# Kernel optimization log

Hardware: AMD Instinct MI355X
Metric: run time of the kernel (lower is better)

The kernel has to match this reference:

```python
import jax, jax.numpy as jnp
import numpy as np

DIM = 64; N_LAYER = 2; B = 2048; M = 64
N_ENT = 100000; N_REL = 200
TEMP = 0.2; KGE_W = 1e-6
MIN_N = 1e-15; BND = 1e-5


def _norm(x):
    return jnp.sqrt(jnp.clip((x * x).sum(-1, keepdims=True), MIN_N))


def _l2(x):
    # F.normalize(p=2): x / max(||x||, 1e-12)
    return x / jnp.maximum(jnp.sqrt((x * x).sum(-1, keepdims=True)), 1e-12)


def _artanh(x):
    return jnp.arctanh(jnp.clip(x, -1.0 + BND, 1.0 - BND))


def expmap0(u):
    n = _norm(u)
    return jnp.tanh(n) * u / n


def logmap0(x):
    n = _norm(x)
    return _artanh(n) * x / n


def mobius_add(x, y):
    x2 = (x * x).sum(-1, keepdims=True)
    y2 = (y * y).sum(-1, keepdims=True)
    xy = (x * y).sum(-1, keepdims=True)
    num = (1 + 2 * xy + y2) * x + (1 - x2) * y
    den = 1 + 2 * xy + x2 * y2
    return num / jnp.clip(den, MIN_N)


def expmap(u, p):
    lam = 2.0 / jnp.clip(1.0 - (p * p).sum(-1, keepdims=True), MIN_N)
    n = _norm(u)
    return mobius_add(p, jnp.tanh(lam * n / 2.0) * u / n)


def logmap(x, p):
    m = mobius_add(-p, x)
    n = _norm(m)
    lam = 2.0 / jnp.clip(1.0 - (p * p).sum(-1, keepdims=True), MIN_N)
    return (2.0 / lam) * _artanh(n) * m / n


def _ed_agg(h, path, t, att_w1, att_w2):
    # attention: Linear(2d,d,no bias) -> LeakyReLU(0)==ReLU -> Linear(d,1,no bias) -> Sigmoid
    x = jnp.concatenate([h, path], -1)                       # [B,M,2d]
    a = jax.nn.sigmoid(jax.nn.relu(x @ att_w1) @ att_w2)[..., 0]  # [B,M]
    w = jax.nn.softmax(a, axis=-1)
    return (w[..., None] * t).sum(1)                          # [B,d]


def _hyper_agg(h, path, t, curvature, a2_w1, a2_b1, a2_w2, a2_b2):
    h, path, t = _l2(h), _l2(path), _l2(t)
    hh = expmap0(h) * jnp.abs(curvature)
    ht = expmap(t, hh)
    hr = expmap(path, hh)
    tang = logmap0(jnp.concatenate([hh, hr], -1))            # [B,M,2d]
    a = jnp.tanh(jax.nn.relu(tang @ a2_w1 + a2_b1) @ a2_w2 + a2_b2)[..., 0]
    w = jax.nn.softmax(a, axis=-1)                            # [B,M]
    agg = w[..., None] * ht
    mean_pt = (w[..., None] * hh).sum(1, keepdims=True)       # [B,1,d]
    e = logmap(agg, mean_pt)
    return (w[..., None] * e).sum(1)                          # [B,d]


def _build(E, R, h_idx, r_idx, t_idx, init_emb, agg):
    embs = [init_emb]
    for i in range(N_LAYER):
        h = E[h_idx[0]]
        path = R[r_idx[0]]
        for k in range(1, i + 1):  # faithful to source: inner loop reuses index i
            h = h + E[h_idx[i]]
            path = path * R[r_idx[i]]
        embs.append(agg(h, path, E[t_idx[i]]))
    return jnp.stack(embs)  # [L+1, B, d]


def _mlcl(a_stack, b_stack):
    # vectorized over layer index i of MLCL_Loss(a[i], b[i], a_list, b_list)
    na, nb = _l2(a_stack), _l2(b_stack)                       # [L+1,B,d]
    d = na.shape[-1]
    pos = (na * nb).sum(-1)                                   # [L+1,B]
    ttl1 = jnp.einsum('lbd,md->lbm', na, nb.reshape(-1, d))
    ttl2 = jnp.einsum('lbd,md->lbm', nb, na.reshape(-1, d))
    ep = jnp.exp(pos / TEMP)
    l1 = -jnp.log(ep / jnp.exp(ttl1 / TEMP).sum(-1)).sum()
    l2 = -jnp.log(ep / jnp.exp(ttl2 / TEMP).sum(-1)).sum()
    return KGE_W * (l1 + l2)


def _cat_rev(stack):
    # e = stack[0]; for i in 1..L: e = cat(stack[i], e) -> [L, L-1, ..., 0]
    return jnp.concatenate([stack[i] for i in range(stack.shape[0] - 1, -1, -1)], -1)


def setup_inputs() -> dict:
    key = jax.random.key(0)
    ks = jax.random.split(key, 24)
    def ent_idx(k):
        return jax.random.randint(k, (N_LAYER, B, M), 0, N_ENT, dtype=jnp.int32)
    def rel_idx(k):
        return jax.random.randint(k, (N_LAYER, B, M), 0, N_REL, dtype=jnp.int32)
    inp = {
        'items': jax.random.randint(ks[0], (B,), 0, N_ENT, dtype=jnp.int32),
        'ucf_h': ent_idx(ks[1]), 'ucf_r': rel_idx(ks[2]), 'ucf_t': ent_idx(ks[3]),
        'ikg_h': ent_idx(ks[4]), 'ikg_r': rel_idx(ks[5]), 'ikg_t': ent_idx(ks[6]),
        'ukg_h': ent_idx(ks[7]), 'ukg_r': rel_idx(ks[8]), 'ukg_t': ent_idx(ks[9]),
        'icf_h': ent_idx(ks[10]), 'icf_r': rel_idx(ks[11]), 'icf_t': ent_idx(ks[12]),
        'ent_emb': jax.random.normal(ks[13], (N_ENT, DIM), jnp.float32) * 0.02,
        'rel_emb': jax.random.normal(ks[14], (N_REL, DIM), jnp.float32) * 0.02,
        'att_w1': jax.random.normal(ks[15], (2 * DIM, DIM), jnp.float32) * 0.05,
        'att_w2': jax.random.normal(ks[16], (DIM, 1), jnp.float32) * 0.05,
        'att2_w1': jax.random.normal(ks[17], (2 * DIM, DIM), jnp.float32) * 0.05,
        'att2_b1': jnp.zeros((DIM,), jnp.float32),
        'att2_w2': jax.random.normal(ks[18], (DIM, 1), jnp.float32) * 0.05,
        'att2_b2': jnp.zeros((1,), jnp.float32),
        'curvature': jnp.asarray(1.0, jnp.float32),
    }
    return inp


def reference(items, ucf_h, ucf_r, ucf_t, ikg_h, ikg_r, ikg_t,
              ukg_h, ukg_r, ukg_t, icf_h, icf_r, icf_t,
              ent_emb, rel_emb, att_w1, att_w2,
              att2_w1, att2_b1, att2_w2, att2_b2, curvature):
    ed = lambda h, p, t: _ed_agg(h, p, t, att_w1, att_w2)
    hy = lambda h, p, t: _hyper_agg(h, p, t, curvature, att2_w1, att2_b1, att2_w2, att2_b2)
    ucf = _build(ent_emb, rel_emb, ucf_h, ucf_r, ucf_t, ent_emb[ucf_h[0]].mean(1), ed)
    ikg = _build(ent_emb, rel_emb, ikg_h, ikg_r, ikg_t, ent_emb[items], ed)
    ukg = _build(ent_emb, rel_emb, ukg_h, ukg_r, ukg_t, ent_emb[ukg_h[0]].mean(1), hy)
    icf = _build(ent_emb, rel_emb, icf_h, icf_r, icf_t, ent_emb[icf_h[0]].mean(1), hy)
    kge_loss = _mlcl(ucf, ukg) + _mlcl(ikg, icf)
    e_u = jnp.concatenate([_cat_rev(ucf), _cat_rev(ukg)], -1)
    e_i = jnp.concatenate([_cat_rev(icf), _cat_rev(ikg)], -1)
    scores = jax.nn.sigmoid((e_i * e_u).sum(-1))
    return scores, kge_loss
```

## Files before the change

### kernel.cpp

```cpp
#include <hip/hip_runtime.h>
#include <hip/hip_bf16.h>
#include <cstdint>
#include <cstddef>

constexpr int NB = 2048;
constexpr int NM = 64;
constexpr int ND = 64;
constexpr int NBM = NB * NM;
constexpr int NROWS = 3 * NB;
constexpr int STACK = 3 * NB * ND;
constexpr int NZ = 8;

typedef __attribute__((ext_vector_type(8))) short short8;
typedef __attribute__((ext_vector_type(4))) float float4v;

__device__ __forceinline__ float wsum(float v) {
#pragma unroll
  for (int o = 32; o > 0; o >>= 1) v += __shfl_xor(v, o, 64);
  return v;
}

__device__ __forceinline__ float wmax(float v) {
#pragma unroll
  for (int o = 32; o > 0; o >>= 1) v = fmaxf(v, __shfl_xor(v, o, 64));
  return v;
}

__device__ __forceinline__ float rcpf(float x) { return __builtin_amdgcn_rcpf(x); }
__device__ __forceinline__ float sqf(float x) { return __builtin_amdgcn_sqrtf(x); }

__device__ __forceinline__ float fast_tanh(float x) {
  float t = __expf(2.f * x);
  return (t - 1.f) * rcpf(t + 1.f);
}

__device__ __forceinline__ float artanh_clip(float x) {
  x = fminf(fmaxf(x, -1.f + 1e-5f), 1.f - 1e-5f);
  return 0.5f * __logf((1.f + x) * rcpf(1.f - x));
}

__device__ __forceinline__ ushort f2bf(float f) {
  return (ushort)((__float_as_uint(f) + 0x8000u) >> 16);
}
__device__ __forceinline__ float bf2f(ushort u) {
  return __uint_as_float((uint)u << 16);
}
__device__ __forceinline__ uint pack_bf2(float h, float p) {
  uint hu = __float_as_uint(h) + 0x8000u;
  uint pu = __float_as_uint(p) + 0x8000u;
  return __builtin_amdgcn_perm(pu, hu, 0x07060302);
}
__device__ __forceinline__ float hp_lo(uint v) { return __uint_as_float(v << 16); }
__device__ __forceinline__ float hp_hi(uint v) { return __uint_as_float(v & 0xFFFF0000u); }

__device__ __forceinline__ float readlane_f(float v, int l) {
  return __int_as_float(__builtin_amdgcn_readlane(__float_as_int(v), l));
}

__global__ __launch_bounds__(256) void pack_w1_kernel(
    const float* __restrict__ w1, ushort* __restrict__ out) {
  int e = blockIdx.x * 256 + threadIdx.x;
  if (e >= 8192) return;
  int j = e & 7, ln = (e >> 3) & 63, nt = (e >> 9) & 3, kt = e >> 11;
  int n = nt * 16 + (ln & 15), k = kt * 32 + ((ln >> 4) << 3) + j;
  out[e] = f2bf(w1[k * 64 + n]);
}

__global__ __launch_bounds__(64) void init_item_kernel(
    const float* __restrict__ E, const int* __restrict__ idx, float* __restrict__ out) {
  int b = blockIdx.x, lane = threadIdx.x;
  out[(size_t)b * ND + lane] = E[(size_t)idx[b] * ND + lane];
}

constexpr int OFF_H = 0;
constexpr int OFF_P = 4608;
constexpr int OFF_T = 9728;
constexpr int XS = 152;
constexpr int REGA_SZ = 14336;

__global__ __launch_bounds__(256) void agg_all_kernel(
    const float* __restrict__ E, const float* __restrict__ R,
    const int* __restrict__ h0, const int* __restrict__ r0, const int* __restrict__ t0,
    const int* __restrict__ h1, const int* __restrict__ r1, const int* __restrict__ t1,
    const int* __restrict__ h2, const int* __restrict__ r2, const int* __restrict__ t2,
    const int* __restrict__ h3, const int* __restrict__ r3, const int* __restrict__ t3,
    const ushort* __restrict__ w1p_ed, const float* __restrict__ w2_ed,
    const ushort* __restrict__ w1p_hy, const float* __restrict__ b1,
    const float* __restrict__ w2_hy, const float* __restrict__ b2,
    const float* __restrict__ curv,
    float* __restrict__ s_ucf, float* __restrict__ s_ikg,
    float* __restrict__ s_ukg, float* __restrict__ s_icf) {
  __shared__ __align__(16) ushort regA[REGA_SZ];
  __shared__ float a_s[64];
  __shared__ float part[4][64];
  __shared__ float minit[4][64];

  const int b = blockIdx.x;
  const int fam = blockIdx.y;
  const int tid = threadIdx.x;
  const int wave = tid >> 6, lane = tid & 63;
  const int m0 = __builtin_amdgcn_readfirstlane(wave) * 16;
  const int colq = lane & 15, quad = lane >> 4;
  const size_t L = (size_t)NB * ND;

  const int* h_idx = (fam == 0) ? h0 : (fam == 1) ? h1 : (fam == 2) ? h2 : h3;
  const int* r_idx = (fam == 0) ? r0 : (fam == 1) ? r1 : (fam == 2) ? r2 : r3;
  const int* t_idx = (fam == 0) ? t0 : (fam == 1) ? t1 : (fam == 2) ? t2 : t3;
  float* sb = (fam == 0) ? s_ucf : (fam == 1) ? s_ikg : (fam == 2) ? s_ukg : s_icf;

  uint hp[16];

  if (fam < 2) {
    const int do_init = (fam == 0);
    for (int layer = 0; layer < 2; ++layer) {
      float tv[16];
      if (layer == 0) {
        float macc = 0.f;
#pragma unroll
        for (int mi = 0; mi < 16; ++mi) {
          const int m = m0 + mi;
          float hd = E[(size_t)h_idx[b * NM + m] * ND + lane];
          float pd = R[(size_t)r_idx[b * NM + m] * ND + lane];
          macc += hd;
          uint pk = pack_bf2(hd, pd);
          hp[mi] = pk;
          regA[m * XS + lane] = (ushort)pk;
          regA[m * XS + 64 + lane] = (ushort)(pk >> 16);
        }
        if (do_init) minit[wave][lane] = macc;
      } else {
#pragma unroll
        for (int mi = 0; mi < 16; ++mi) {
          const int m = m0 + mi;
          float hd = hp_lo(hp[mi]) + E[(size_t)h_idx[NBM + b * NM + m] * ND + lane];
          float pd = hp_hi(hp[mi]) * R[(size_t)r_idx[NBM + b * NM + m] * ND + lane];
          uint pk = pack_bf2(hd, pd);
          hp[mi] = pk;
          regA[m * XS + lane] = (ushort)pk;
          regA[m * XS + 64 + lane] = (ushort)(pk >> 16);
        }
      }
#pragma unroll
      for (int mi = 0; mi < 16; ++mi)
        tv[mi] = E[(size_t)t_idx[(size_t)layer * NBM + b * NM + m0 + mi] * ND + lane];

      {
        short8 afr[4];
#pragma unroll
        for (int kt = 0; kt < 4; ++kt)
          afr[kt] = *(const short8*)&regA[(m0 + colq) * XS + kt * 32 + quad * 8];
        float w2v[4];
#pragma unroll
        for (int nt = 0; nt < 4; ++nt) w2v[nt] = w2_ed[nt * 16 + colq];
        float cc[4][4];
#pragma unroll
        for (int nt = 0; nt < 4; ++nt) {
          float4v c = {0.f, 0.f, 0.f, 0.f};
#pragma unroll
          for (int kt = 0; kt < 4; ++kt) {
            short8 bfr = *(const short8*)&w1p_ed[(((kt << 2) | nt) * 64 + lane) * 8];
            c = __builtin_amdgcn_mfma_f32_16x16x32_bf16(afr[kt], bfr, c, 0, 0, 0);
          }
#pragma unroll
          for (int i = 0; i < 4; ++i) cc[nt][i] = c[i];
        }
        float sred[4];
#pragma unroll
        for (int i = 0; i < 4; ++i)
          sred[i] = fmaxf(cc[0][i], 0.f) * w2v[0] + fmaxf(cc[1][i], 0.f) * w2v[1] +
                    fmaxf(cc[2][i], 0.f) * w2v[2] + fmaxf(cc[3][i], 0.f) * w2v[3];
#pragma unroll
        for (int o = 8; o > 0; o >>= 1) {
#pragma unroll
          for (int i = 0; i < 4; ++i) sred[i] += __shfl_xor(sred[i], o, 64);
        }
        if (colq == 0) {
#pragma unroll
          for (int i = 0; i < 4; ++i)
            a_s[m0 + quad * 4 + i] = 1.f / (1.f + __expf(-sred[i]));
        }
      }
      __syncthreads();

      float wl;
      {
        float v = a_s[lane];
        float mx = wmax(v);
        float e = __expf(v - mx);
        wl = e / wsum(e);
      }
      if (layer == 0 && do_init && wave == 0)
        sb[(size_t)b * ND + lane] =
            (minit[0][lane] + minit[1][lane] + minit[2][lane] + minit[3][lane]) * (1.f / 64.f);

      float o = 0.f;
#pragma unroll
      for (int mi = 0; mi < 16; ++mi)
        o = fmaf(readlane_f(wl, m0 + mi), tv[mi], o);
      part[wave][lane] = o;
      __syncthreads();
      if (wave == 0)
        sb[(layer + 1) * L + (size_t)b * ND + lane] =
            part[0][lane] + part[1][lane] + part[2][lane] + part[3][lane];
    }
  } else {
    const float cabs = fabsf(*curv);
    const int j = colq;
    const int srcl = ((j >> 2) << 4) + j;

    for (int layer = 0; layer < 2; ++layer) {
      if (layer == 0) {
        float macc = 0.f;
#pragma unroll
        for (int mi = 0; mi < 16; ++mi) {
          const int m = m0 + mi;
          float hd = E[(size_t)h_idx[b * NM + m] * ND + lane];
          float pd = R[(size_t)r_idx[b * NM + m] * ND + lane];
          float td = E[(size_t)t_idx[b * NM + m] * ND + lane];
          macc += hd;
          uint pk = pack_bf2(hd, pd);
          hp[mi] = pk;
          regA[OFF_H + m * 72 + lane] = (ushort)pk;
          regA[OFF_P + m * 72 + lane] = (ushort)(pk >> 16);
          regA[OFF_T + m * 72 + lane] = f2bf(td);
        }
        part[wave][lane] = macc;
      } else {
#pragma unroll
        for (int mi = 0; mi < 16; ++mi) {
          const int m = m0 + mi;
          float hd = hp_lo(hp[mi]) + E[(size_t)h_idx[NBM + b * NM + m] * ND + lane];
          float pd = hp_hi(hp[mi]) * R[(size_t)r_idx[NBM + b * NM + m] * ND + lane];
          float td = E[(size_t)t_idx[(size_t)NBM + b * NM + m] * ND + lane];
          uint pk = pack_bf2(hd, pd);
          hp[mi] = pk;
          regA[OFF_H + m * 72 + lane] = (ushort)pk;
          regA[OFF_P + m * 72 + lane] = (ushort)(pk >> 16);
          regA[OFF_T + m * 72 + lane] = f2bf(td);
        }
      }

      float sh, sp, st, sht, shp;
      {
        const int fr = m0 + colq;
        const ushort* pH = &regA[OFF_H + fr * 72 + quad * 8];
        const ushort* pP = &regA[OFF_P + fr * 72 + quad * 8];
        const ushort* pT = &regA[OFF_T + fr * 72 + quad * 8];
        short8 hh0 = *(const short8*)pH, hh1 = *(const short8*)(pH + 32);
        short8 pp0 = *(const short8*)pP, pp1 = *(const short8*)(pP + 32);
        short8 tt0 = *(const short8*)pT, tt1 = *(const short8*)(pT + 32);
        const int dr = colq & 3;
#define DIAG_DOT(OUTV, A0, A1, B0, B1)                                      \
        {                                                                    \
          float4v c = {0.f, 0.f, 0.f, 0.f};                                  \
          c = __builtin_amdgcn_mfma_f32_16x16x32_bf16(A0, B0, c, 0, 0, 0);   \
          c = __builtin_amdgcn_mfma_f32_16x16x32_bf16(A1, B1, c, 0, 0, 0);   \
          float dv = (dr & 2) ? ((dr & 1) ? c[3] : c[2])                     \
                              : ((dr & 1) ? c[1] : c[0]);                    \
          OUTV = __shfl(dv, srcl, 64);                                       \
        }
        DIAG_DOT(sh, hh0, hh1, hh0, hh1)
        DIAG_DOT(sp, pp0, pp1, pp0, pp1)
        DIAG_DOT(st, tt0, tt1, tt0, tt1)
        DIAG_DOT(sht, hh0, hh1, tt0, tt1)
        DIAG_DOT(shp, hh0, hh1, pp0, pp1)
#undef DIAG_DOT
      }

      float g_ch, g_e1, g_e2, g_gh, g_q1, g_q2, g_hts2;
      {
        float rih = rcpf(fmaxf(sqf(sh), 1e-12f));
        float rip = rcpf(fmaxf(sqf(sp), 1e-12f));
        float rit = rcpf(fmaxf(sqf(st), 1e-12f));
        float nh = sqf(fmaxf(sh * rih * rih, 1e-15f));
        float ch = fast_tanh(nh) * rcpf(nh) * rih * cabs;
        float p2 = ch * ch * sh;
        float lam = 2.f * rcpf(fmaxf(1.f - p2, 1e-15f));
        float ntn = sqf(fmaxf(st * rit * rit, 1e-15f));
        float ct = fast_tanh(0.5f * lam * ntn) * rcpf(ntn) * rit;
        float y2 = ct * ct * st, xy = ch * ct * sht;
        float At = 1.f + 2.f * xy + y2, Bt = 1.f - p2;
        float rdt = rcpf(fmaxf(1.f + 2.f * xy + p2 * y2, 1e-15f));
        g_e1 = At * ch * rdt;
        g_e2 = Bt * ct * rdt;
        g_hts2 = g_e1 * g_e1 * sh + 2.f * g_e1 * g_e2 * sht + g_e2 * g_e2 * st;
        float npn = sqf(fmaxf(sp * rip * rip, 1e-15f));
        float cp = fast_tanh(0.5f * lam * npn) * rcpf(npn) * rip;
        float z2 = cp * cp * sp, xz = ch * cp * shp;
        float Ar = 1.f + 2.f * xz + z2;
        float rdr = rcpf(fmaxf(1.f + 2.f * xz + p2 * z2, 1e-15f));
        float f1 = Ar * ch * rdr, f2 = Bt * cp * rdr;
        float hr2 = f1 * f1 * sh + 2.f * f1 * f2 * shp + f2 * f2 * sp;
        float n128 = sqf(fmaxf(p2 + hr2, 1e-15f));
        float fq = artanh_clip(n128) * rcpf(n128);
        g_ch = ch;
        g_gh = fq * ch;
        g_q1 = fq * f1;
        g_q2 = fq * f2;
      }

      __syncthreads();
      if (layer == 0 && wave == 0)
        sb[(size_t)b * ND + lane] =
            (part[0][lane] + part[1][lane] + part[2][lane] + part[3][lane]) * (1.f / 64.f);

#pragma unroll
      for (int mi = 0; mi < 16; ++mi) {
        const int m = m0 + mi;
        float hvf = hp_lo(hp[mi]);
        float pvf = hp_hi(hp[mi]);
        float tvf = bf2f(regA[OFF_T + m * 72 + lane]);
        float ghm = readlane_f(g_gh, mi);
        float q1m = readlane_f(g_q1, mi);
        float q2m = readlane_f(g_q2, mi);
        float e1m = readlane_f(g_e1, mi);
        float e2m = readlane_f(g_e2, mi);
        regA[m * XS + lane] = f2bf(ghm * hvf);
        regA[m * XS + 64 + lane] = f2bf(q1m * hvf + q2m * pvf);
        regA[OFF_T + m * 72 + lane] = f2bf(e1m * hvf + e2m * tvf);
      }

      {
        short8 afr[4];
#pragma unroll
        for (int kt = 0; kt < 4; ++kt)
          afr[kt] = *(const short8*)&regA[(m0 + colq) * XS + kt * 32 + quad * 8];
        float b1v[4], w2v[4];
#pragma unroll
        for (int nt = 0; nt < 4; ++nt) {
          b1v[nt] = b1[nt * 16 + colq];
          w2v[nt] = w2_hy[nt * 16 + colq];
        }
        float cc[4][4];
#pragma unroll
        for (int nt = 0; nt < 4; ++nt) {
          float4v c = {0.f, 0.f, 0.f, 0.f};
#pragma unroll
          for (int kt = 0; kt < 4; ++kt) {
            short8 bfr = *(const short8*)&w1p_hy[(((kt << 2) | nt) * 64 + lane) * 8];
            c = __builtin_amdgcn_mfma_f32_16x16x32_bf16(afr[kt], bfr, c, 0, 0, 0);
          }
#pragma unroll
          for (int i = 0; i < 4; ++i) cc[nt][i] = c[i];
        }
        float b2v = b2[0];
        float sred[4];
#pragma unroll
        for (int i = 0; i < 4; ++i)
          sred[i] = fmaxf(cc[0][i] + b1v[0], 0.f) * w2v[0] +
                    fmaxf(cc[1][i] + b1v[1], 0.f) * w2v[1] +
                    fmaxf(cc[2][i] + b1v[2], 0.f) * w2v[2] +
                    fmaxf(cc[3][i] + b1v[3], 0.f) * w2v[3];
#pragma unroll
        for (int o = 8; o > 0; o >>= 1) {
#pragma unroll
          for (int i = 0; i < 4; ++i) sred[i] += __shfl_xor(sred[i], o, 64);
        }
        if (colq == 0) {
#pragma unroll
          for (int i = 0; i < 4; ++i)
            a_s[m0 + quad * 4 + i] = fast_tanh(sred[i] + b2v);
        }
      }
      __syncthreads();

      float wl;
      {
        float v = a_s[lane];
        float mx = wmax(v);
        float e = __expf(v - mx);
        wl = e / wsum(e);
      }

      float mp = 0.f;
#pragma unroll
      for (int mi = 0; mi < 16; ++mi)
        mp = fmaf(readlane_f(wl, m0 + mi) * readlane_f(g_ch, mi), hp_lo(hp[mi]), mp);
      part[wave][lane] = mp;
      __syncthreads();

      float mv = part[0][lane] + part[1][lane] + part[2][lane] + part[3][lane];
      float p2m = wsum(mv * mv);

      float dpv;
      {
        const ushort* pA = &regA[OFF_T + (m0 + colq) * 72 + quad * 8];
        short8 a0 = *(const short8*)pA, a1 = *(const short8*)(pA + 32);
        short8 bm0, bm1;
#pragma unroll
        for (int jj = 0; jj < 8; ++jj) {
          bm0[jj] = (short)f2bf(__shfl(mv, quad * 8 + jj, 64));
          bm1[jj] = (short)f2bf(__shfl(mv, 32 + quad * 8 + jj, 64));
        }
        float4v c = {0.f, 0.f, 0.f, 0.f};
        c = __builtin_amdgcn_mfma_f32_16x16x32_bf16(a0, bm0, c, 0, 0, 0);
        c = __builtin_amdgcn_mfma_f32_16x16x32_bf16(a1, bm1, c, 0, 0, 0);
        const int dr = colq & 3;
        float dv = (dr & 2) ? ((dr & 1) ? c[3] : c[2]) : ((dr & 1) ? c[1] : c[0]);
        dpv = __shfl(dv, srcl, 64);
      }

      const float be = fmaxf(1.f - p2m, 1e-15f);
      float g1, g2;
      {
        float wm = __shfl(wl, m0 + j, 64);
        float y2 = wm * wm * g_hts2;
        float xy = -wm * dpv;
        float al = 1.f + 2.f * xy + y2;
        float rd = rcpf(fmaxf(1.f + 2.f * xy + p2m * y2, 1e-15f));
        float md2 = (al * al * p2m - 2.f * al * be * wm * dpv + be * be * y2) * rd * rd;
        float n = sqf(fmaxf(md2, 1e-15f));
        float sm = be * artanh_clip(n) * rcpf(n) * rd;
        g1 = wm * wm * sm * be;
        g2 = wm * sm * al;
      }
      float ovec = 0.f, cA = 0.f;
#pragma unroll
      for (int mi = 0; mi < 16; ++mi) {
        const int m = m0 + mi;
        float htf = bf2f(regA[OFF_T + m * 72 + lane]);
        ovec = fmaf(readlane_f(g1, mi), htf, ovec);
        cA += readlane_f(g2, mi);
      }
      part[wave][lane] = ovec - cA * mv;
      __syncthreads();
      if (wave == 0)
        sb[(layer + 1) * L + (size_t)b * ND + lane] =
            part[0][lane] + part[1][lane] + part[2][lane] + part[3][lane];
    }
  }
}

__global__ __launch_bounds__(256) void l2pos_kernel(
    const float* __restrict__ stacks, __hip_bfloat16* __restrict__ nbf,
    float* __restrict__ pos) {
  int row = blockIdx.x * 4 + (threadIdx.x >> 6);
  int lane = threadIdx.x & 63;
  int sa = blockIdx.y, sb = sa + 2;
  size_t offa = (size_t)sa * STACK + (size_t)row * ND + lane;
  size_t offb = (size_t)sb * STACK + (size_t)row * ND + lane;
  float a = stacks[offa];
  float c = stacks[offb];
  float q0 = a * a, q1 = c * c, q2 = a * c;
#pragma unroll
  for (int o = 32; o > 0; o >>= 1) {
    q0 += __shfl_xor(q0, o, 64);
    q1 += __shfl_xor(q1, o, 64);
    q2 += __shfl_xor(q2, o, 64);
  }
  float ra = rcpf(fmaxf(sqf(q0), 1e-12f));
  float rc = rcpf(fmaxf(sqf(q1), 1e-12f));
  ushort ua = f2bf(a * ra), uc = f2bf(c * rc);
  nbf[offa] = *(__hip_bfloat16*)&ua;
  nbf[offb] = *(__hip_bfloat16*)&uc;
  if (lane == 0) pos[sa * NROWS + row] = q2 * ra * rc;
}

__global__ __launch_bounds__(256) void lse_mfma_kernel(
    const ushort* __restrict__ nbf, float* __restrict__ Spart) {
  __shared__ __align__(16) ushort ytile[2][64 * 72];
  const int tid = threadIdx.x;
  const int wave = tid >> 6, lane = tid & 63;
  const int pair = blockIdx.y;
  const int z = blockIdx.z;
  int xi = (pair & 2) ? ((pair & 1) ? 3 : 1) : ((pair & 1) ? 2 : 0);
  int yi = xi ^ 2;
  const ushort* X = nbf + (size_t)xi * STACK;
  const ushort* Y = nbf + (size_t)yi * STACK;
  const int r0 = blockIdx.x * 64 + wave * 16;
  const int row = lane & 15, quad = lane >> 4;

  short8 a0 = *(const short8*)&X[(size_t)(r0 + row) * 64 + quad * 8];
  short8 a1 = *(const short8*)&X[(size_t)(r0 + row) * 64 + 32 + quad * 8];

  const int srow = tid >> 2, schunk = tid & 3;
  constexpr int NT = (NROWS / NZ) / 64;
  const int c0 = z * (NROWS / NZ);
  const ushort* sg = &Y[(size_t)(c0 + srow) * 64 + schunk * 16];
  ushort* sl = &ytile[0][0] + srow * 72 + schunk * 16;

  {
    short8 s0 = *(const short8*)sg;
    short8 s1 = *(const short8*)(sg + 8);
    *(short8*)sl = s0;
    *(short8*)(sl + 8) = s1;
  }
  __syncthreads();

  float rsum[4] = {0.f, 0.f, 0.f, 0.f};
  for (int ct = 0; ct < NT; ++ct) {
    const int cur = ct & 1;
    short8 n0, n1;
    if (ct + 1 < NT) {
      const ushort* src = sg + (size_t)(ct + 1) * 64 * 64;
      n0 = *(const short8*)src;
      n1 = *(const short8*)(src + 8);
    }
#pragma unroll
    for (int nt = 0; nt < 4; ++nt) {
      const ushort* yr = &ytile[cur][(nt * 16 + row) * 72 + quad * 8];
      short8 b0 = *(const short8*)yr;
      short8 b1 = *(const short8*)(yr + 32);
      float4v c = {0.f, 0.f, 0.f, 0.f};
      c = __builtin_amdgcn_mfma_f32_16x16x32_bf16(a0, b0, c, 0, 0, 0);
      c = __builtin_amdgcn_mfma_f32_16x16x32_bf16(a1, b1, c, 0, 0, 0);
#pragma unroll
      for (int i = 0; i < 4; ++i) rsum[i] += __expf(c[i] * 5.f);
    }
    if (ct + 1 < NT) {
      ushort* dst = &ytile[0][0] + ((ct + 1) & 1) * (64 * 72) + srow * 72 + schunk * 16;
      *(short8*)dst = n0;
      *(short8*)(dst + 8) = n1;
      __syncthreads();
    }
  }
#pragma unroll
  for (int i = 0; i < 4; ++i) {
    float v = rsum[i];
    v += __shfl_xor(v, 1, 64);
    v += __shfl_xor(v, 2, 64);
    v += __shfl_xor(v, 4, 64);
    v += __shfl_xor(v, 8, 64);
    if (row == 0)
      Spart[((size_t)z * 4 + pair) * NROWS + r0 + quad * 4 + i] = v;
  }
}

__global__ __launch_bounds__(256) void scores_kernel(
    const float* __restrict__ stacks, float* __restrict__ out) {
  int b = blockIdx.x * 4 + (threadIdx.x >> 6);
  int lane = threadIdx.x & 63;
  float s = 0.f;
#pragma unroll
  for (int l = 0; l < 3; ++l) {
    size_t o = (size_t)l * NB * ND + (size_t)b * ND + lane;
    s += stacks[0 * (size_t)STACK + o] * stacks[3 * (size_t)STACK + o]
       + stacks[2 * (size_t)STACK + o] * stacks[1 * (size_t)STACK + o];
  }
  s = wsum(s);
  if (lane == 0) out[b] = 1.f / (1.f + __expf(-s));
}

__global__ __launch_bounds__(256) void loss_part_kernel(
    const float* __restrict__ Spart, const float* __restrict__ pos,
    double* __restrict__ lossp) {
  __shared__ double red[256];
  const int t = threadIdx.x, blk = blockIdx.x;
  double acc = 0.0;
#pragma unroll
  for (int r = 0; r < 2; ++r) {
    int i = blk * 512 + r * 256 + t;
    float s = 0.f;
#pragma unroll
    for (int zz = 0; zz < NZ; ++zz) s += Spart[i + zz * 4 * NROWS];
    acc += (double)__logf(s);
  }
  {
    int jj = blk * 256 + t;
    acc -= 10.0 * (double)pos[jj];
  }
  red[t] = acc;
  __syncthreads();
  for (int s = 128; s > 0; s >>= 1) {
    if (t < s) red[t] += red[t + s];
    __syncthreads();
  }
  if (t == 0) lossp[blk] = red[0];
}

__global__ __launch_bounds__(64) void loss_final_kernel(
    const double* __restrict__ lossp, float* __restrict__ out) {
  int lane = threadIdx.x;
  double v = (lane < 48) ? lossp[lane] : 0.0;
#pragma unroll
  for (int o = 32; o > 0; o >>= 1) v += __shfl_xor(v, o, 64);
  if (lane == 0) out[NB] = (float)(1e-6 * v);
}

extern "C" void kernel_launch(void* const* d_in, const int* in_sizes, int n_in,
                              void* d_out, int out_size, void* d_ws, size_t ws_size,
                              hipStream_t stream) {
  const int* items = (const int*)d_in[0];
  const int* ucf_h = (const int*)d_in[1];
  const int* ucf_r = (const int*)d_in[2];
  const int* ucf_t = (const int*)d_in[3];
  const int* ikg_h = (const int*)d_in[4];
  const int* ikg_r = (const int*)d_in[5];
  const int* ikg_t = (const int*)d_in[6];
  const int* ukg_h = (const int*)d_in[7];
  const int* ukg_r = (const int*)d_in[8];
  const int* ukg_t = (const int*)d_in[9];
  const int* icf_h = (const int*)d_in[10];
  const int* icf_r = (const int*)d_in[11];
  const int* icf_t = (const int*)d_in[12];
  const float* E = (const float*)d_in[13];
  const float* R = (const float*)d_in[14];
  const float* att_w1 = (const float*)d_in[15];
  const float* att_w2 = (const float*)d_in[16];
  const float* a2_w1 = (const float*)d_in[17];
  const float* a2_b1 = (const float*)d_in[18];
  const float* a2_w2 = (const float*)d_in[19];
  const float* a2_b2 = (const float*)d_in[20];
  const float* curv = (const float*)d_in[21];
  float* outp = (float*)d_out;

  float* ws = (float*)d_ws;
  float* stacks = ws;
  float* Spart = stacks + 4 * (size_t)STACK;
  float* posarr = Spart + (size_t)NZ * 4 * NROWS;
  __hip_bfloat16* nbf = (__hip_bfloat16*)(posarr + 2 * (size_t)NROWS);
  ushort* w1p_ed = (ushort*)(nbf + 4 * (size_t)STACK);
  ushort* w1p_hy = w1p_ed + 8192;
  double* lossp = (double*)(w1p_hy + 8192);

  float* ucf = stacks + 0 * (size_t)STACK;
  float* ikg = stacks + 1 * (size_t)STACK;
  float* ukg = stacks + 2 * (size_t)STACK;
  float* icf = stacks + 3 * (size_t)STACK;

  pack_w1_kernel<<<32, 256, 0, stream>>>(att_w1, w1p_ed);
  pack_w1_kernel<<<32, 256, 0, stream>>>(a2_w1, w1p_hy);

  init_item_kernel<<<NB, 64, 0, stream>>>(E, items, ikg);

  agg_all_kernel<<<dim3(NB, 4), 256, 0, stream>>>(
      E, R,
      ucf_h, ucf_r, ucf_t, ikg_h, ikg_r, ikg_t,
      ukg_h, ukg_r, ukg_t, icf_h, icf_r, icf_t,
      w1p_ed, att_w2, w1p_hy, a2_b1, a2_w2, a2_b2, curv,
      ucf, ikg, ukg, icf);

  l2pos_kernel<<<dim3(NROWS / 4, 2), 256, 0, stream>>>(stacks, nbf, posarr);
  lse_mfma_kernel<<<dim3(NROWS / 64, 4, NZ), 256, 0, stream>>>((const ushort*)nbf, Spart);

  scores_kernel<<<NB / 4, 256, 0, stream>>>(stacks, outp);
  loss_part_kernel<<<48, 256, 0, stream>>>(Spart, posarr, lossp);
  loss_final_kernel<<<1, 64, 0, stream>>>(lossp, outp);
}
```

Measured before the change: 345.0 us.

## Fuse L2 normalization into aggregation and merge small prep/score kernels

Each aggregated row now has its bf16 L2-normalized copy written directly at the end of the aggregation kernel, which removes the separate l2pos pass over the stacks. The two weight-packing kernels and the item init kernel are merged into one prep kernel, and the pos-dot and scores kernels are merged into one launch. The aggregation grid is swapped to (fam, b) so blocks for the four families of the same batch row run near each other. The pos dot product is now computed from bf16-normalized values instead of fp32, a small precision change.

```diff
diff --git a/kernel.cpp b/kernel.cpp
--- a/kernel.cpp
+++ b/kernel.cpp
@@ -57,19 +57,32 @@
   return __int_as_float(__builtin_amdgcn_readlane(__float_as_int(v), l));
 }
 
-__global__ __launch_bounds__(256) void pack_w1_kernel(
-    const float* __restrict__ w1, ushort* __restrict__ out) {
-  int e = blockIdx.x * 256 + threadIdx.x;
-  if (e >= 8192) return;
-  int j = e & 7, ln = (e >> 3) & 63, nt = (e >> 9) & 3, kt = e >> 11;
-  int n = nt * 16 + (ln & 15), k = kt * 32 + ((ln >> 4) << 3) + j;
-  out[e] = f2bf(w1[k * 64 + n]);
-}
-
-__global__ __launch_bounds__(64) void init_item_kernel(
-    const float* __restrict__ E, const int* __restrict__ idx, float* __restrict__ out) {
-  int b = blockIdx.x, lane = threadIdx.x;
-  out[(size_t)b * ND + lane] = E[(size_t)idx[b] * ND + lane];
+__device__ __forceinline__ void write_row_norm(
+    float v, float* __restrict__ frow, ushort* __restrict__ nrow, int lane) {
+  float nv = wsum(v * v);
+  float r = rcpf(fmaxf(sqf(nv), 1e-12f));
+  frow[lane] = v;
+  nrow[lane] = f2bf(v * r);
+}
+
+__global__ __launch_bounds__(64) void prep_kernel(
+    const float* __restrict__ E, const int* __restrict__ items,
+    const float* __restrict__ w1_ed, const float* __restrict__ w1_hy,
+    float* __restrict__ s_ikg, ushort* __restrict__ nbf_ikg,
+    ushort* __restrict__ w1p_ed, ushort* __restrict__ w1p_hy) {
+  int blk = blockIdx.x, lane = threadIdx.x;
+  if (blk < NB) {
+    float v = E[(size_t)items[blk] * ND + lane];
+    write_row_norm(v, s_ikg + (size_t)blk * ND, nbf_ikg + (size_t)blk * ND, lane);
+  } else {
+    int e = (blk - NB) * 64 + lane;
+    const float* w1 = (e < 8192) ? w1_ed : w1_hy;
+    ushort* out = (e < 8192) ? w1p_ed : w1p_hy;
+    e &= 8191;
+    int j = e & 7, ln = (e >> 3) & 63, nt = (e >> 9) & 3, kt = e >> 11;
+    int n = nt * 16 + (ln & 15), k = kt * 32 + ((ln >> 4) << 3) + j;
+    out[e] = f2bf(w1[k * 64 + n]);
+  }
 }
 
 constexpr int OFF_H = 0;
@@ -88,15 +101,14 @@
     const ushort* __restrict__ w1p_hy, const float* __restrict__ b1,
     const float* __restrict__ w2_hy, const float* __restrict__ b2,
     const float* __restrict__ curv,
-    float* __restrict__ s_ucf, float* __restrict__ s_ikg,
-    float* __restrict__ s_ukg, float* __restrict__ s_icf) {
+    float* __restrict__ stacks, ushort* __restrict__ nbf) {
   __shared__ __align__(16) ushort regA[REGA_SZ];
   __shared__ float a_s[64];
   __shared__ float part[4][64];
   __shared__ float minit[4][64];
 
-  const int b = blockIdx.x;
-  const int fam = blockIdx.y;
+  const int fam = blockIdx.x;
+  const int b = blockIdx.y;
   const int tid = threadIdx.x;
   const int wave = tid >> 6, lane = tid & 63;
   const int m0 = __builtin_amdgcn_readfirstlane(wave) * 16;
@@ -106,7 +118,8 @@
   const int* h_idx = (fam == 0) ? h0 : (fam == 1) ? h1 : (fam == 2) ? h2 : h3;
   const int* r_idx = (fam == 0) ? r0 : (fam == 1) ? r1 : (fam == 2) ? r2 : r3;
   const int* t_idx = (fam == 0) ? t0 : (fam == 1) ? t1 : (fam == 2) ? t2 : t3;
-  float* sb = (fam == 0) ? s_ucf : (fam == 1) ? s_ikg : (fam == 2) ? s_ukg : s_icf;
+  float* sb = stacks + (size_t)fam * STACK;
+  ushort* nb = nbf + (size_t)fam * STACK;
 
   uint hp[16];
 
@@ -189,9 +202,10 @@
         float e = __expf(v - mx);
         wl = e / wsum(e);
       }
-      if (layer == 0 && do_init && wave == 0)
-        sb[(size_t)b * ND + lane] =
-            (minit[0][lane] + minit[1][lane] + minit[2][lane] + minit[3][lane]) * (1.f / 64.f);
+      if (layer == 0 && do_init && wave == 0) {
+        float v = (minit[0][lane] + minit[1][lane] + minit[2][lane] + minit[3][lane]) * (1.f / 64.f);
+        write_row_norm(v, sb + (size_t)b * ND, nb + (size_t)b * ND, lane);
+      }
 
       float o = 0.f;
 #pragma unroll
@@ -199,9 +213,11 @@
         o = fmaf(readlane_f(wl, m0 + mi), tv[mi], o);
       part[wave][lane] = o;
       __syncthreads();
-      if (wave == 0)
-        sb[(layer + 1) * L + (size_t)b * ND + lane] =
-            part[0][lane] + part[1][lane] + part[2][lane] + part[3][lane];
+      if (wave == 0) {
+        float v = part[0][lane] + part[1][lane] + part[2][lane] + part[3][lane];
+        write_row_norm(v, sb + (layer + 1) * L + (size_t)b * ND,
+                       nb + (layer + 1) * L + (size_t)b * ND, lane);
+      }
     }
   } else {
     const float cabs = fabsf(*curv);
@@ -300,9 +316,10 @@
       }
 
       __syncthreads();
-      if (layer == 0 && wave == 0)
-        sb[(size_t)b * ND + lane] =
-            (part[0][lane] + part[1][lane] + part[2][lane] + part[3][lane]) * (1.f / 64.f);
+      if (layer == 0 && wave == 0) {
+        float v = (part[0][lane] + part[1][lane] + part[2][lane] + part[3][lane]) * (1.f / 64.f);
+        write_row_norm(v, sb + (size_t)b * ND, nb + (size_t)b * ND, lane);
+      }
 
 #pragma unroll
       for (int mi = 0; mi < 16; ++mi) {
@@ -424,36 +441,40 @@
       }
       part[wave][lane] = ovec - cA * mv;
       __syncthreads();
-      if (wave == 0)
-        sb[(layer + 1) * L + (size_t)b * ND + lane] =
-            part[0][lane] + part[1][lane] + part[2][lane] + part[3][lane];
+      if (wave == 0) {
+        float v = part[0][lane] + part[1][lane] + part[2][lane] + part[3][lane];
+        write_row_norm(v, sb + (layer + 1) * L + (size_t)b * ND,
+                       nb + (layer + 1) * L + (size_t)b * ND, lane);
+      }
     }
   }
 }
 
-__global__ __launch_bounds__(256) void l2pos_kernel(
-    const float* __restrict__ stacks, __hip_bfloat16* __restrict__ nbf,
-    float* __restrict__ pos) {
-  int row = blockIdx.x * 4 + (threadIdx.x >> 6);
+__global__ __launch_bounds__(256) void pos_scores_kernel(
+    const ushort* __restrict__ nbf, const float* __restrict__ stacks,
+    float* __restrict__ pos, float* __restrict__ out) {
   int lane = threadIdx.x & 63;
-  int sa = blockIdx.y, sb = sa + 2;
-  size_t offa = (size_t)sa * STACK + (size_t)row * ND + lane;
-  size_t offb = (size_t)sb * STACK + (size_t)row * ND + lane;
-  float a = stacks[offa];
-  float c = stacks[offb];
-  float q0 = a * a, q1 = c * c, q2 = a * c;
-#pragma unroll
-  for (int o = 32; o > 0; o >>= 1) {
-    q0 += __shfl_xor(q0, o, 64);
-    q1 += __shfl_xor(q1, o, 64);
-    q2 += __shfl_xor(q2, o, 64);
-  }
-  float ra = rcpf(fmaxf(sqf(q0), 1e-12f));
-  float rc = rcpf(fmaxf(sqf(q1), 1e-12f));
-  ushort ua = f2bf(a * ra), uc = f2bf(c * rc);
-  nbf[offa] = *(__hip_bfloat16*)&ua;
-  nbf[offb] = *(__hip_bfloat16*)&uc;
-  if (lane == 0) pos[sa * NROWS + row] = q2 * ra * rc;
+  int wave = threadIdx.x >> 6;
+  if (blockIdx.y < 2) {
+    int row = blockIdx.x * 4 + wave;
+    int sa = blockIdx.y;
+    float a = bf2f(nbf[(size_t)sa * STACK + (size_t)row * ND + lane]);
+    float c = bf2f(nbf[(size_t)(sa + 2) * STACK + (size_t)row * ND + lane]);
+    float d = wsum(a * c);
+    if (lane == 0) pos[sa * NROWS + row] = d;
+  } else {
+    int b = blockIdx.x * 4 + wave;
+    if (b >= NB) return;
+    float s = 0.f;
+#pragma unroll
+    for (int l = 0; l < 3; ++l) {
+      size_t o = (size_t)l * NB * ND + (size_t)b * ND + lane;
+      s += stacks[0 * (size_t)STACK + o] * stacks[3 * (size_t)STACK + o]
+         + stacks[2 * (size_t)STACK + o] * stacks[1 * (size_t)STACK + o];
+    }
+    s = wsum(s);
+    if (lane == 0) out[b] = 1.f / (1.f + __expf(-s));
+  }
 }
 
 __global__ __launch_bounds__(256) void lse_mfma_kernel(
@@ -524,21 +545,6 @@
     if (row == 0)
       Spart[((size_t)z * 4 + pair) * NROWS + r0 + quad * 4 + i] = v;
   }
-}
-
-__global__ __launch_bounds__(256) void scores_kernel(
-    const float* __restrict__ stacks, float* __restrict__ out) {
-  int b = blockIdx.x * 4 + (threadIdx.x >> 6);
-  int lane = threadIdx.x & 63;
-  float s = 0.f;
-#pragma unroll
-  for (int l = 0; l < 3; ++l) {
-    size_t o = (size_t)l * NB * ND + (size_t)b * ND + lane;
-    s += stacks[0 * (size_t)STACK + o] * stacks[3 * (size_t)STACK + o]
-       + stacks[2 * (size_t)STACK + o] * stacks[1 * (size_t)STACK + o];
-  }
-  s = wsum(s);
-  if (lane == 0) out[b] = 1.f / (1.f + __expf(-s));
 }
 
 __global__ __launch_bounds__(256) void loss_part_kernel(
@@ -608,32 +614,27 @@
   float* stacks = ws;
   float* Spart = stacks + 4 * (size_t)STACK;
   float* posarr = Spart + (size_t)NZ * 4 * NROWS;
-  __hip_bfloat16* nbf = (__hip_bfloat16*)(posarr + 2 * (size_t)NROWS);
-  ushort* w1p_ed = (ushort*)(nbf + 4 * (size_t)STACK);
+  ushort* nbf = (ushort*)(posarr + 2 * (size_t)NROWS);
+  ushort* w1p_ed = nbf + 4 * (size_t)STACK;
   ushort* w1p_hy = w1p_ed + 8192;
   double* lossp = (double*)(w1p_hy + 8192);
 
-  float* ucf = stacks + 0 * (size_t)STACK;
   float* ikg = stacks + 1 * (size_t)STACK;
-  float* ukg = stacks + 2 * (size_t)STACK;
-  float* icf = stacks + 3 * (size_t)STACK;
-
-  pack_w1_kernel<<<32, 256, 0, stream>>>(att_w1, w1p_ed);
-  pack_w1_kernel<<<32, 256, 0, stream>>>(a2_w1, w1p_hy);
-
-  init_item_kernel<<<NB, 64, 0, stream>>>(E, items, ikg);
-
-  agg_all_kernel<<<dim3(NB, 4), 256, 0, stream>>>(
+  ushort* nbf_ikg = nbf + 1 * (size_t)STACK;
+
+  prep_kernel<<<NB + 256, 64, 0, stream>>>(E, items, att_w1, a2_w1,
+                                           ikg, nbf_ikg, w1p_ed, w1p_hy);
+
+  agg_all_kernel<<<dim3(4, NB), 256, 0, stream>>>(
       E, R,
       ucf_h, ucf_r, ucf_t, ikg_h, ikg_r, ikg_t,
       ukg_h, ukg_r, ukg_t, icf_h, icf_r, icf_t,
       w1p_ed, att_w2, w1p_hy, a2_b1, a2_w2, a2_b2, curv,
-      ucf, ikg, ukg, icf);
-
-  l2pos_kernel<<<dim3(NROWS / 4, 2), 256, 0, stream>>>(stacks, nbf, posarr);
-  lse_mfma_kernel<<<dim3(NROWS / 64, 4, NZ), 256, 0, stream>>>((const ushort*)nbf, Spart);
-
-  scores_kernel<<<NB / 4, 256, 0, stream>>>(stacks, outp);
+      stacks, nbf);
+
+  pos_scores_kernel<<<dim3(NROWS / 4, 3), 256, 0, stream>>>(nbf, stacks, posarr, outp);
+  lse_mfma_kernel<<<dim3(NROWS / 64, 4, NZ), 256, 0, stream>>>(nbf, Spart);
+
   loss_part_kernel<<<48, 256, 0, stream>>>(Spart, posarr, lossp);
   loss_final_kernel<<<1, 64, 0, stream>>>(lossp, outp);
 }
```

After: 392.2 us. 1.14x slower.
